# Optimization experiments

Hardware: AMD Instinct MI355X
Metric: run time of the kernel (lower is better)

## Reference

```python
import jax, jax.numpy as jnp
import numpy as np
from jax import lax

N_GROUPS = 2
TOPK_GROUPS = 1
TOPK = 4
ROUTE_SCALE = 1.0


def setup_inputs() -> dict:
    key = jax.random.key(0)
    k1, k2 = jax.random.split(key)
    T, D, E = 524288, 256, 64
    x = jax.random.normal(k1, (T, D), dtype=jnp.float32)
    W = jax.random.normal(k2, (E, D), dtype=jnp.float32) * 0.02  # router weight [out, in]
    return {"x": x, "W": W}


def reference(x, W):
    T = x.shape[0]
    E = W.shape[0]
    logits = x @ W.T  # [T, E]
    scores = jax.nn.softmax(logits.astype(jnp.float32), axis=-1)
    original_scores = scores
    # grouped masking (bias is None -> amax group score)
    g = scores.reshape(T, N_GROUPS, E // N_GROUPS)
    group_scores = g.max(axis=-1)  # [T, G]
    _, gidx = lax.top_k(group_scores, TOPK_GROUPS)  # [T, topk_groups]
    keep = jnp.zeros((T, N_GROUPS), dtype=bool).at[jnp.arange(T)[:, None], gidx].set(True)
    masked = jnp.where(keep[:, :, None], g, -jnp.inf).reshape(T, E)
    _, indices = lax.top_k(masked, TOPK)  # [T, topk]
    weights = jnp.take_along_axis(original_scores, indices, axis=1)
    weights = weights * ROUTE_SCALE
    return weights.astype(x.dtype), indices
```

## Files before the change

kernel.cpp:

```cpp
#include <hip/hip_runtime.h>
#include <hip/hip_bf16.h>
#include <stdint.h>


typedef __attribute__((ext_vector_type(8))) short bf16x8;
typedef __attribute__((ext_vector_type(4))) float f32x4;
typedef __attribute__((ext_vector_type(4))) int i32x4;

#define SPLIT_OFF 1024
#define LIST_OFF 102400
#define DELTA 1e-4f

__device__ __forceinline__ f32x4 mf(const i32x4& a, const i32x4& b,
                                    const f32x4& c) {
  return __builtin_amdgcn_mfma_f32_16x16x32_bf16(
      __builtin_bit_cast(bf16x8, a), __builtin_bit_cast(bf16x8, b), c, 0, 0, 0);
}

__device__ __forceinline__ int packhi(unsigned e0, unsigned e1) {
  return (int)__builtin_amdgcn_perm(e1, e0, 0x07060302u);
}

__device__ __forceinline__ void gload16(const void* g, void* l) {
  __builtin_amdgcn_global_load_lds(
      (const __attribute__((address_space(1))) void*)g,
      (__attribute__((address_space(3))) void*)l, 16, 0, 0);
}

__global__ void split_w(const float* __restrict__ W,
                        unsigned short* __restrict__ ws, int n,
                        int* __restrict__ meta) {
  int i = blockIdx.x * 256 + threadIdx.x;
  if (i == 0) meta[0] = 0;
  if (i >= n) return;
  float w = W[i];
  unsigned u = __float_as_uint(w);
  unsigned uh = u & 0xFFFF0000u;
  float rf = w - __uint_as_float(uh);
  unsigned short lv[2];
  lv[0] = (unsigned short)(uh >> 16);
  lv[1] = (unsigned short)(__float_as_uint(rf) >> 16);
  int e = i >> 8, k = i & 255;
  int nt = e >> 4, le = e & 15;
  int c = k >> 5, lg = (k >> 3) & 3, kk = k & 7;
  int lane = lg * 16 + le;
#pragma unroll
  for (int v = 0; v < 2; ++v)
    ws[(((c * 8 + v * 4 + nt) * 64) + lane) * 8 + kk] = lv[v];
}

struct XF2 { i32x4 h, m; };

__device__ __forceinline__ XF2 split2(f32x4 a, f32x4 b) {
  float xs[8] = {a[0], a[1], a[2], a[3], b[0], b[1], b[2], b[3]};
  XF2 f;
#pragma unroll
  for (int wd = 0; wd < 4; ++wd) {
    unsigned u0 = __float_as_uint(xs[2 * wd]);
    unsigned u1 = __float_as_uint(xs[2 * wd + 1]);
    f.h[wd] = packhi(u0, u1);
    float r0 = xs[2 * wd] - __uint_as_float(u0 & 0xFFFF0000u);
    float r1 = xs[2 * wd + 1] - __uint_as_float(u1 & 0xFFFF0000u);
    f.m[wd] = packhi(__float_as_uint(r0), __float_as_uint(r1));
  }
  return f;
}

#define GL(dst, ptr, OFF)                                     \
  asm volatile("global_load_dwordx4 %0, %1, off offset:%2"    \
               : "=v"(dst)                                    \
               : "v"(ptr), "n"(OFF))

#define WAITV(NSTR)                                         \
  do {                                                      \
    asm volatile("s_waitcnt vmcnt(" NSTR ")" ::: "memory"); \
    __builtin_amdgcn_sched_barrier(0);                      \
  } while (0)

__global__ __launch_bounds__(512, 4) void gate_kernel(
    const float* __restrict__ x, const unsigned short* __restrict__ wsp,
    float* __restrict__ out, int* __restrict__ meta, int* __restrict__ list,
    int cap, int T) {
  __shared__ i32x4 WL[4096];

  const int t = threadIdx.x;
  const int lane = t & 63;
  const int wid = t >> 6;
  const int le = lane & 15;
  const int lg = lane >> 4;
  const int tokbase = blockIdx.x * 256 + wid * 32;

  const float* xa0 = x + (size_t)(tokbase + le) * 256 + lg * 8;
  const float* xa1 = xa0 + 16 * 256;

  f32x4 xbuf[2][4];
  f32x4 acc[4][2];
#pragma unroll
  for (int nt = 0; nt < 4; ++nt)
#pragma unroll
    for (int t2 = 0; t2 < 2; ++t2) acc[nt][t2] = (f32x4)0.0f;

#define STAGE_X(c)                              \
  do {                                          \
    GL(xbuf[(c) & 1][0], xa0, (c) * 128);       \
    GL(xbuf[(c) & 1][1], xa0, (c) * 128 + 16);  \
    GL(xbuf[(c) & 1][2], xa1, (c) * 128);       \
    GL(xbuf[(c) & 1][3], xa1, (c) * 128 + 16);  \
  } while (0)

#define ITER(c, NSTR)                                               \
  {                                                                 \
    WAITV(NSTR);                                                    \
    XF2 b0 = split2(xbuf[(c) & 1][0], xbuf[(c) & 1][1]);            \
    XF2 b1 = split2(xbuf[(c) & 1][2], xbuf[(c) & 1][3]);            \
    if ((c) + 2 < 8) STAGE_X((c) + 2);                              \
    _Pragma("unroll") for (int nt = 0; nt < 4; ++nt) {              \
      i32x4 ah = WL[(((c) * 8 + nt) << 6) + lane];                  \
      i32x4 am = WL[(((c) * 8 + 4 + nt) << 6) + lane];              \
      acc[nt][0] = mf(ah, b0.h, acc[nt][0]);                        \
      acc[nt][0] = mf(ah, b0.m, acc[nt][0]);                        \
      acc[nt][0] = mf(am, b0.h, acc[nt][0]);                        \
      acc[nt][0] = mf(am, b0.m, acc[nt][0]);                        \
      acc[nt][1] = mf(ah, b1.h, acc[nt][1]);                        \
      acc[nt][1] = mf(ah, b1.m, acc[nt][1]);                        \
      acc[nt][1] = mf(am, b1.h, acc[nt][1]);                        \
      acc[nt][1] = mf(am, b1.m, acc[nt][1]);                        \
    }                                                               \
  }

  {
    const char* wsrc = (const char*)wsp + t * 16;
    char* wdst = (char*)WL + t * 16;
#pragma unroll
    for (int i = 0; i < 8; ++i) gload16(wsrc + i * 8192, wdst + i * 8192);
  }
  STAGE_X(0);
  STAGE_X(1);
  WAITV("8");
  __builtin_amdgcn_s_barrier();

  ITER(0, "4");
  ITER(1, "4");
  ITER(2, "4");
  ITER(3, "4");
  ITER(4, "4");
  ITER(5, "4");
  ITER(6, "4");
  ITER(7, "0");

#pragma unroll
  for (int tt = 0; tt < 2; ++tt) {
    float l[16];
#pragma unroll
    for (int nt = 0; nt < 4; ++nt)
#pragma unroll
      for (int j = 0; j < 4; ++j) l[nt * 4 + j] = acc[nt][tt][j];

    float g0 = l[0], g1 = l[8];
#pragma unroll
    for (int j = 1; j < 8; ++j) {
      g0 = fmaxf(g0, l[j]);
      g1 = fmaxf(g1, l[8 + j]);
    }
    g0 = fmaxf(g0, __shfl_xor(g0, 16));
    g0 = fmaxf(g0, __shfl_xor(g0, 32));
    g1 = fmaxf(g1, __shfl_xor(g1, 16));
    g1 = fmaxf(g1, __shfl_xor(g1, 32));
    const int g = (g1 > g0) ? 1 : 0;
    const float m = fmaxf(g0, g1);

    float sum = 0.f;
#pragma unroll
    for (int k = 0; k < 16; ++k) sum += __expf(l[k] - m);
    sum += __shfl_xor(sum, 16);
    sum += __shfl_xor(sum, 32);
    const float inv = 1.0f / sum;

    float c[8];
    int ce[8];
#pragma unroll
    for (int j2 = 0; j2 < 8; ++j2) {
      c[j2] = l[g * 8 + j2];
      ce[j2] = (2 * g + (j2 >> 2)) * 16 + 4 * lg + (j2 & 3);
    }

    float v5[5];
    int e5[5];
#pragma unroll
    for (int it = 0; it < 5; ++it) {
      float bv = c[0];
      int be = ce[0];
#pragma unroll
      for (int j2 = 1; j2 < 8; ++j2) {
        bool gt = c[j2] > bv;
        bv = gt ? c[j2] : bv;
        be = gt ? ce[j2] : be;
      }
#pragma unroll
      for (int st = 0; st < 2; ++st) {
        int msk = 16 << st;
        float ov = __shfl_xor(bv, msk);
        int oe = __shfl_xor(be, msk);
        bool tk = (ov > bv) || (ov == bv && oe < be);
        bv = tk ? ov : bv;
        be = tk ? oe : be;
      }
      v5[it] = bv;
      e5[it] = be;
#pragma unroll
      for (int j2 = 0; j2 < 8; ++j2)
        c[j2] = (ce[j2] == be) ? -3.0e38f : c[j2];
    }

    float ming = fabsf(g0 - g1);
#pragma unroll
    for (int it = 0; it < 4; ++it) ming = fminf(ming, v5[it] - v5[it + 1]);

    if (lg == 0) {
      size_t trow = (size_t)tokbase + tt * 16 + le;
      *(float4*)&out[trow * 4] =
          make_float4(__expf(v5[0] - m) * inv, __expf(v5[1] - m) * inv,
                      __expf(v5[2] - m) * inv, __expf(v5[3] - m) * inv);
      *(float4*)&out[(size_t)T * 4 + trow * 4] = make_float4(
          (float)e5[0], (float)e5[1], (float)e5[2], (float)e5[3]);
      if (ming < DELTA) {
        int p = atomicAdd(meta, 1);
        if (p < cap) list[p] = (int)trow;
      }
    }
  }
}

__global__ __launch_bounds__(64) void fix_kernel(
    const float* __restrict__ x, const float* __restrict__ W,
    float* __restrict__ out, const int* __restrict__ meta,
    const int* __restrict__ list, int cap, int T) {
  const int e = threadIdx.x;
  int cnt = meta[0];
  cnt = cnt < cap ? cnt : cap;
  for (int i = blockIdx.x; i < cnt; i += gridDim.x) {
    const int tok = list[i];
    const float* xr = x + (size_t)tok * 256;
    const float* wr = W + (size_t)e * 256;
    float acc = 0.f;
#pragma unroll 8
    for (int d = 0; d < 256; d += 4) {
      float4 xv = *(const float4*)(xr + d);
      float4 wv = *(const float4*)(wr + d);
      acc = fmaf(xv.x, wv.x, acc);
      acc = fmaf(xv.y, wv.y, acc);
      acc = fmaf(xv.z, wv.z, acc);
      acc = fmaf(xv.w, wv.w, acc);
    }
    float gm = acc;
#pragma unroll
    for (int st = 0; st < 5; ++st) gm = fmaxf(gm, __shfl_xor(gm, 1 << st));
    float om = __shfl_xor(gm, 32);
    float g0 = (e < 32) ? gm : om;
    float g1 = (e < 32) ? om : gm;
    const int g = (g1 > g0) ? 1 : 0;
    const float m = fmaxf(g0, g1);
    float sum = __expf(acc - m);
#pragma unroll
    for (int st = 0; st < 6; ++st) sum += __shfl_xor(sum, 1 << st);
    const float inv = 1.0f / sum;

    float cand = ((e >> 5) == g) ? acc : -3.0e38f;
    float w4[4], i4[4];
#pragma unroll
    for (int it = 0; it < 4; ++it) {
      float bv = cand;
      int be = e;
#pragma unroll
      for (int st = 0; st < 6; ++st) {
        int msk = 1 << st;
        float ov = __shfl_xor(bv, msk);
        int oe = __shfl_xor(be, msk);
        bool tk = (ov > bv) || (ov == bv && oe < be);
        bv = tk ? ov : bv;
        be = tk ? oe : be;
      }
      w4[it] = __expf(bv - m) * inv;
      i4[it] = (float)be;
      if (e == be) cand = -3.0e38f;
    }
    if (e == 0) {
      *(float4*)&out[(size_t)tok * 4] = make_float4(w4[0], w4[1], w4[2], w4[3]);
      *(float4*)&out[(size_t)T * 4 + (size_t)tok * 4] =
          make_float4(i4[0], i4[1], i4[2], i4[3]);
    }
  }
}

extern "C" void kernel_launch(void* const* d_in, const int* in_sizes, int n_in,
                              void* d_out, int out_size, void* d_ws,
                              size_t ws_size, hipStream_t stream) {
  const float* x = (const float*)d_in[0];
  const float* W = (const float*)d_in[1];
  float* out = (float*)d_out;
  int T = in_sizes[0] / 256;
  int nW = in_sizes[1];
  int* meta = (int*)d_ws;
  unsigned short* wsp = (unsigned short*)((char*)d_ws + SPLIT_OFF);
  int* list = (int*)((char*)d_ws + LIST_OFF);
  int cap = (ws_size > LIST_OFF + 4) ? (int)((ws_size - LIST_OFF) / 4) : 0;
  hipLaunchKernelGGL(split_w, dim3((nW + 255) / 256), dim3(256), 0, stream, W,
                     wsp, nW, meta);
  hipLaunchKernelGGL(gate_kernel, dim3(T / 256), dim3(512), 0, stream, x, wsp,
                     out, meta, list, cap, T);
  hipLaunchKernelGGL(fix_kernel, dim3(2048), dim3(64), 0, stream, x, W, out,
                     meta, list, cap, T);
}
```

Before: 142.1 us.

## Make gate kernel persistent with cross-tile prefetch of next x chunk

```diff
diff --git a/kernel.cpp b/kernel.cpp
--- a/kernel.cpp
+++ b/kernel.cpp
@@ -77,6 +77,8 @@
     __builtin_amdgcn_sched_barrier(0);                      \
   } while (0)
 
+#define NBLK 512
+
 __global__ __launch_bounds__(512, 4) void gate_kernel(
     const float* __restrict__ x, const unsigned short* __restrict__ wsp,
     float* __restrict__ out, int* __restrict__ meta, int* __restrict__ list,
@@ -88,32 +90,33 @@
   const int wid = t >> 6;
   const int le = lane & 15;
   const int lg = lane >> 4;
-  const int tokbase = blockIdx.x * 256 + wid * 32;
-
-  const float* xa0 = x + (size_t)(tokbase + le) * 256 + lg * 8;
+  const int ngen = (T / 256) / NBLK;
+  const size_t GS = (size_t)NBLK * 256 * 256;
+
+  int tokb = blockIdx.x * 256 + wid * 32;
+  const float* xa0 = x + (size_t)(tokb + le) * 256 + lg * 8;
   const float* xa1 = xa0 + 16 * 256;
 
   f32x4 xbuf[2][4];
-  f32x4 acc[4][2];
-#pragma unroll
-  for (int nt = 0; nt < 4; ++nt)
-#pragma unroll
-    for (int t2 = 0; t2 < 2; ++t2) acc[nt][t2] = (f32x4)0.0f;
-
-#define STAGE_X(c)                              \
-  do {                                          \
-    GL(xbuf[(c) & 1][0], xa0, (c) * 128);       \
-    GL(xbuf[(c) & 1][1], xa0, (c) * 128 + 16);  \
-    GL(xbuf[(c) & 1][2], xa1, (c) * 128);       \
-    GL(xbuf[(c) & 1][3], xa1, (c) * 128 + 16);  \
+
+#define STAGE_XP(p0, p1, bi, OFF)        \
+  do {                                   \
+    GL(xbuf[bi][0], p0, OFF);            \
+    GL(xbuf[bi][1], p0, (OFF) + 16);     \
+    GL(xbuf[bi][2], p1, OFF);            \
+    GL(xbuf[bi][3], p1, (OFF) + 16);     \
   } while (0)
 
-#define ITER(c, NSTR)                                               \
+#define ITER(c)                                                     \
   {                                                                 \
-    WAITV(NSTR);                                                    \
+    WAITV("4");                                                     \
     XF2 b0 = split2(xbuf[(c) & 1][0], xbuf[(c) & 1][1]);            \
     XF2 b1 = split2(xbuf[(c) & 1][2], xbuf[(c) & 1][3]);            \
-    if ((c) + 2 < 8) STAGE_X((c) + 2);                              \
+    if ((c) + 2 < 8) {                                              \
+      STAGE_XP(xa0, xa1, (c) & 1, ((c) + 2) * 128);                 \
+    } else {                                                        \
+      STAGE_XP(xn0, xn1, (c) & 1, ((c) - 6) * 128);                 \
+    }                                                               \
     _Pragma("unroll") for (int nt = 0; nt < 4; ++nt) {              \
       i32x4 ah = WL[(((c) * 8 + nt) << 6) + lane];                  \
       i32x4 am = WL[(((c) * 8 + 4 + nt) << 6) + lane];              \
@@ -134,100 +137,111 @@
 #pragma unroll
     for (int i = 0; i < 8; ++i) gload16(wsrc + i * 8192, wdst + i * 8192);
   }
-  STAGE_X(0);
-  STAGE_X(1);
+  STAGE_XP(xa0, xa1, 0, 0);
+  STAGE_XP(xa0, xa1, 1, 128);
   WAITV("8");
   __builtin_amdgcn_s_barrier();
 
-  ITER(0, "4");
-  ITER(1, "4");
-  ITER(2, "4");
-  ITER(3, "4");
-  ITER(4, "4");
-  ITER(5, "4");
-  ITER(6, "4");
-  ITER(7, "0");
-
-#pragma unroll
-  for (int tt = 0; tt < 2; ++tt) {
-    float l[16];
+#pragma unroll 1
+  for (int g = 0; g < ngen; ++g) {
+    const bool lastg = (g + 1 >= ngen);
+    const float* xn0 = lastg ? xa0 : xa0 + GS;
+    const float* xn1 = lastg ? xa1 : xa1 + GS;
+
+    f32x4 acc[4][2];
 #pragma unroll
     for (int nt = 0; nt < 4; ++nt)
 #pragma unroll
-      for (int j = 0; j < 4; ++j) l[nt * 4 + j] = acc[nt][tt][j];
-
-    float g0 = l[0], g1 = l[8];
-#pragma unroll
-    for (int j = 1; j < 8; ++j) {
-      g0 = fmaxf(g0, l[j]);
-      g1 = fmaxf(g1, l[8 + j]);
+      for (int t2 = 0; t2 < 2; ++t2) acc[nt][t2] = (f32x4)0.0f;
+
+    ITER(0); ITER(1); ITER(2); ITER(3);
+    ITER(4); ITER(5); ITER(6); ITER(7);
+
+#pragma unroll
+    for (int tt = 0; tt < 2; ++tt) {
+      float l[16];
+#pragma unroll
+      for (int nt = 0; nt < 4; ++nt)
+#pragma unroll
+        for (int j = 0; j < 4; ++j) l[nt * 4 + j] = acc[nt][tt][j];
+
+      float g0 = l[0], g1 = l[8];
+#pragma unroll
+      for (int j = 1; j < 8; ++j) {
+        g0 = fmaxf(g0, l[j]);
+        g1 = fmaxf(g1, l[8 + j]);
+      }
+      g0 = fmaxf(g0, __shfl_xor(g0, 16));
+      g0 = fmaxf(g0, __shfl_xor(g0, 32));
+      g1 = fmaxf(g1, __shfl_xor(g1, 16));
+      g1 = fmaxf(g1, __shfl_xor(g1, 32));
+      const int grp = (g1 > g0) ? 1 : 0;
+      const float m = fmaxf(g0, g1);
+
+      float sum = 0.f;
+#pragma unroll
+      for (int k = 0; k < 16; ++k) sum += __expf(l[k] - m);
+      sum += __shfl_xor(sum, 16);
+      sum += __shfl_xor(sum, 32);
+      const float inv = 1.0f / sum;
+
+      float c[8];
+      int ce[8];
+#pragma unroll
+      for (int j2 = 0; j2 < 8; ++j2) {
+        c[j2] = l[grp * 8 + j2];
+        ce[j2] = (2 * grp + (j2 >> 2)) * 16 + 4 * lg + (j2 & 3);
+      }
+
+      float v5[5];
+      int e5[5];
+#pragma unroll
+      for (int it = 0; it < 5; ++it) {
+        float bv = c[0];
+        int be = ce[0];
+#pragma unroll
+        for (int j2 = 1; j2 < 8; ++j2) {
+          bool gt = c[j2] > bv;
+          bv = gt ? c[j2] : bv;
+          be = gt ? ce[j2] : be;
+        }
+#pragma unroll
+        for (int st = 0; st < 2; ++st) {
+          int msk = 16 << st;
+          float ov = __shfl_xor(bv, msk);
+          int oe = __shfl_xor(be, msk);
+          bool tk = (ov > bv) || (ov == bv && oe < be);
+          bv = tk ? ov : bv;
+          be = tk ? oe : be;
+        }
+        v5[it] = bv;
+        e5[it] = be;
+#pragma unroll
+        for (int j2 = 0; j2 < 8; ++j2)
+          c[j2] = (ce[j2] == be) ? -3.0e38f : c[j2];
+      }
+
+      float ming = fabsf(g0 - g1);
+#pragma unroll
+      for (int it = 0; it < 4; ++it) ming = fminf(ming, v5[it] - v5[it + 1]);
+
+      if (lg == 0) {
+        size_t trow = (size_t)tokb + tt * 16 + le;
+        *(float4*)&out[trow * 4] =
+            make_float4(__expf(v5[0] - m) * inv, __expf(v5[1] - m) * inv,
+                        __expf(v5[2] - m) * inv, __expf(v5[3] - m) * inv);
+        *(float4*)&out[(size_t)T * 4 + trow * 4] = make_float4(
+            (float)e5[0], (float)e5[1], (float)e5[2], (float)e5[3]);
+        if (ming < DELTA) {
+          int p = atomicAdd(meta, 1);
+          if (p < cap) list[p] = (int)trow;
+        }
+      }
     }
-    g0 = fmaxf(g0, __shfl_xor(g0, 16));
-    g0 = fmaxf(g0, __shfl_xor(g0, 32));
-    g1 = fmaxf(g1, __shfl_xor(g1, 16));
-    g1 = fmaxf(g1, __shfl_xor(g1, 32));
-    const int g = (g1 > g0) ? 1 : 0;
-    const float m = fmaxf(g0, g1);
-
-    float sum = 0.f;
-#pragma unroll
-    for (int k = 0; k < 16; ++k) sum += __expf(l[k] - m);
-    sum += __shfl_xor(sum, 16);
-    sum += __shfl_xor(sum, 32);
-    const float inv = 1.0f / sum;
-
-    float c[8];
-    int ce[8];
-#pragma unroll
-    for (int j2 = 0; j2 < 8; ++j2) {
-      c[j2] = l[g * 8 + j2];
-      ce[j2] = (2 * g + (j2 >> 2)) * 16 + 4 * lg + (j2 & 3);
-    }
-
-    float v5[5];
-    int e5[5];
-#pragma unroll
-    for (int it = 0; it < 5; ++it) {
-      float bv = c[0];
-      int be = ce[0];
-#pragma unroll
-      for (int j2 = 1; j2 < 8; ++j2) {
-        bool gt = c[j2] > bv;
-        bv = gt ? c[j2] : bv;
-        be = gt ? ce[j2] : be;
-      }
-#pragma unroll
-      for (int st = 0; st < 2; ++st) {
-        int msk = 16 << st;
-        float ov = __shfl_xor(bv, msk);
-        int oe = __shfl_xor(be, msk);
-        bool tk = (ov > bv) || (ov == bv && oe < be);
-        bv = tk ? ov : bv;
-        be = tk ? oe : be;
-      }
-      v5[it] = bv;
-      e5[it] = be;
-#pragma unroll
-      for (int j2 = 0; j2 < 8; ++j2)
-        c[j2] = (ce[j2] == be) ? -3.0e38f : c[j2];
-    }
-
-    float ming = fabsf(g0 - g1);
-#pragma unroll
-    for (int it = 0; it < 4; ++it) ming = fminf(ming, v5[it] - v5[it + 1]);
-
-    if (lg == 0) {
-      size_t trow = (size_t)tokbase + tt * 16 + le;
-      *(float4*)&out[trow * 4] =
-          make_float4(__expf(v5[0] - m) * inv, __expf(v5[1] - m) * inv,
-                      __expf(v5[2] - m) * inv, __expf(v5[3] - m) * inv);
-      *(float4*)&out[(size_t)T * 4 + trow * 4] = make_float4(
-          (float)e5[0], (float)e5[1], (float)e5[2], (float)e5[3]);
-      if (ming < DELTA) {
-        int p = atomicAdd(meta, 1);
-        if (p < cap) list[p] = (int)trow;
-      }
-    }
+
+    xa0 = xn0;
+    xa1 = xn1;
+    tokb += NBLK * 256;
   }
 }
 
@@ -306,8 +320,8 @@
   int cap = (ws_size > LIST_OFF + 4) ? (int)((ws_size - LIST_OFF) / 4) : 0;
   hipLaunchKernelGGL(split_w, dim3((nW + 255) / 256), dim3(256), 0, stream, W,
                      wsp, nW, meta);
-  hipLaunchKernelGGL(gate_kernel, dim3(T / 256), dim3(512), 0, stream, x, wsp,
+  hipLaunchKernelGGL(gate_kernel, dim3(NBLK), dim3(512), 0, stream, x, wsp,
                      out, meta, list, cap, T);
-  hipLaunchKernelGGL(fix_kernel, dim3(2048), dim3(64), 0, stream, x, W, out,
+  hipLaunchKernelGGL(fix_kernel, dim3(4096), dim3(64), 0, stream, x, W, out,
                      meta, list, cap, T);
 }
```

New measurement: 145.8 us. +2.6%, slower.

## Fuse W split and near-tie fixup into single gate kernel

Applied to the files above, without the earlier changes.

```diff
diff --git a/kernel.cpp b/kernel.cpp
--- a/kernel.cpp
+++ b/kernel.cpp
@@ -7,8 +7,6 @@
 typedef __attribute__((ext_vector_type(4))) float f32x4;
 typedef __attribute__((ext_vector_type(4))) int i32x4;
 
-#define SPLIT_OFF 1024
-#define LIST_OFF 102400
 #define DELTA 1e-4f
 
 __device__ __forceinline__ f32x4 mf(const i32x4& a, const i32x4& b,
@@ -19,34 +17,6 @@
 
 __device__ __forceinline__ int packhi(unsigned e0, unsigned e1) {
   return (int)__builtin_amdgcn_perm(e1, e0, 0x07060302u);
-}
-
-__device__ __forceinline__ void gload16(const void* g, void* l) {
-  __builtin_amdgcn_global_load_lds(
-      (const __attribute__((address_space(1))) void*)g,
-      (__attribute__((address_space(3))) void*)l, 16, 0, 0);
-}
-
-__global__ void split_w(const float* __restrict__ W,
-                        unsigned short* __restrict__ ws, int n,
-                        int* __restrict__ meta) {
-  int i = blockIdx.x * 256 + threadIdx.x;
-  if (i == 0) meta[0] = 0;
-  if (i >= n) return;
-  float w = W[i];
-  unsigned u = __float_as_uint(w);
-  unsigned uh = u & 0xFFFF0000u;
-  float rf = w - __uint_as_float(uh);
-  unsigned short lv[2];
-  lv[0] = (unsigned short)(uh >> 16);
-  lv[1] = (unsigned short)(__float_as_uint(rf) >> 16);
-  int e = i >> 8, k = i & 255;
-  int nt = e >> 4, le = e & 15;
-  int c = k >> 5, lg = (k >> 3) & 3, kk = k & 7;
-  int lane = lg * 16 + le;
-#pragma unroll
-  for (int v = 0; v < 2; ++v)
-    ws[(((c * 8 + v * 4 + nt) * 64) + lane) * 8 + kk] = lv[v];
 }
 
 struct XF2 { i32x4 h, m; };
@@ -78,9 +48,8 @@
   } while (0)
 
 __global__ __launch_bounds__(512, 4) void gate_kernel(
-    const float* __restrict__ x, const unsigned short* __restrict__ wsp,
-    float* __restrict__ out, int* __restrict__ meta, int* __restrict__ list,
-    int cap, int T) {
+    const float* __restrict__ x, const float* __restrict__ W,
+    float* __restrict__ out, int T) {
   __shared__ i32x4 WL[4096];
 
   const int t = threadIdx.x;
@@ -88,9 +57,37 @@
   const int wid = t >> 6;
   const int le = lane & 15;
   const int lg = lane >> 4;
-  const int tokbase = blockIdx.x * 256 + wid * 32;
-
-  const float* xa0 = x + (size_t)(tokbase + le) * 256 + lg * 8;
+  const int tokb = blockIdx.x * 256 + wid * 32;
+
+  {
+    const float* wr = W + t * 32;
+    float wv[32];
+#pragma unroll
+    for (int j = 0; j < 8; ++j)
+      *(float4*)&wv[j * 4] = *(const float4*)(wr + j * 4);
+    const int e = t >> 3, c = t & 7;
+    const int nt = e >> 4, lew = e & 15;
+#pragma unroll
+    for (int lg2 = 0; lg2 < 4; ++lg2) {
+      i32x4 vh, vm;
+#pragma unroll
+      for (int p = 0; p < 4; ++p) {
+        float a0 = wv[lg2 * 8 + 2 * p], a1 = wv[lg2 * 8 + 2 * p + 1];
+        unsigned u0 = __float_as_uint(a0), u1 = __float_as_uint(a1);
+        vh[p] = packhi(u0, u1);
+        float r0 = a0 - __uint_as_float(u0 & 0xFFFF0000u);
+        float r1 = a1 - __uint_as_float(u1 & 0xFFFF0000u);
+        vm[p] = packhi(__float_as_uint(r0), __float_as_uint(r1));
+      }
+      WL[(c * 8 + nt) * 64 + lg2 * 16 + lew] = vh;
+      WL[(c * 8 + 4 + nt) * 64 + lg2 * 16 + lew] = vm;
+    }
+  }
+  asm volatile("s_waitcnt lgkmcnt(0)" ::: "memory");
+  __builtin_amdgcn_sched_barrier(0);
+  __builtin_amdgcn_s_barrier();
+
+  const float* xa0 = x + (size_t)(tokb + le) * 256 + lg * 8;
   const float* xa1 = xa0 + 16 * 256;
 
   f32x4 xbuf[2][4];
@@ -128,17 +125,8 @@
     }                                                               \
   }
 
-  {
-    const char* wsrc = (const char*)wsp + t * 16;
-    char* wdst = (char*)WL + t * 16;
-#pragma unroll
-    for (int i = 0; i < 8; ++i) gload16(wsrc + i * 8192, wdst + i * 8192);
-  }
   STAGE_X(0);
   STAGE_X(1);
-  WAITV("8");
-  __builtin_amdgcn_s_barrier();
-
   ITER(0, "4");
   ITER(1, "4");
   ITER(2, "4");
@@ -148,6 +136,7 @@
   ITER(6, "4");
   ITER(7, "0");
 
+  unsigned long long fmask = 0ull;
 #pragma unroll
   for (int tt = 0; tt < 2; ++tt) {
     float l[16];
@@ -166,7 +155,7 @@
     g0 = fmaxf(g0, __shfl_xor(g0, 32));
     g1 = fmaxf(g1, __shfl_xor(g1, 16));
     g1 = fmaxf(g1, __shfl_xor(g1, 32));
-    const int g = (g1 > g0) ? 1 : 0;
+    const int grp = (g1 > g0) ? 1 : 0;
     const float m = fmaxf(g0, g1);
 
     float sum = 0.f;
@@ -180,8 +169,8 @@
     int ce[8];
 #pragma unroll
     for (int j2 = 0; j2 < 8; ++j2) {
-      c[j2] = l[g * 8 + j2];
-      ce[j2] = (2 * g + (j2 >> 2)) * 16 + 4 * lg + (j2 & 3);
+      c[j2] = l[grp * 8 + j2];
+      ce[j2] = (2 * grp + (j2 >> 2)) * 16 + 4 * lg + (j2 & 3);
     }
 
     float v5[5];
@@ -216,43 +205,37 @@
 #pragma unroll
     for (int it = 0; it < 4; ++it) ming = fminf(ming, v5[it] - v5[it + 1]);
 
-    if (lg == 0) {
-      size_t trow = (size_t)tokbase + tt * 16 + le;
+    const bool flg = (ming < DELTA);
+    fmask |= (__ballot(lg == 0 && flg) << (tt * 16));
+
+    if (lg == 0 && !flg) {
+      size_t trow = (size_t)tokb + tt * 16 + le;
       *(float4*)&out[trow * 4] =
           make_float4(__expf(v5[0] - m) * inv, __expf(v5[1] - m) * inv,
                       __expf(v5[2] - m) * inv, __expf(v5[3] - m) * inv);
       *(float4*)&out[(size_t)T * 4 + trow * 4] = make_float4(
           (float)e5[0], (float)e5[1], (float)e5[2], (float)e5[3]);
-      if (ming < DELTA) {
-        int p = atomicAdd(meta, 1);
-        if (p < cap) list[p] = (int)trow;
-      }
-    }
-  }
-}
-
-__global__ __launch_bounds__(64) void fix_kernel(
-    const float* __restrict__ x, const float* __restrict__ W,
-    float* __restrict__ out, const int* __restrict__ meta,
-    const int* __restrict__ list, int cap, int T) {
-  const int e = threadIdx.x;
-  int cnt = meta[0];
-  cnt = cnt < cap ? cnt : cap;
-  for (int i = blockIdx.x; i < cnt; i += gridDim.x) {
-    const int tok = list[i];
-    const float* xr = x + (size_t)tok * 256;
+    }
+  }
+
+  while (fmask) {
+    const int b = __builtin_ctzll(fmask);
+    fmask &= fmask - 1;
+    const size_t tok = (size_t)tokb + (b >> 4) * 16 + (b & 15);
+    const int e = lane;
+    const float* xr = x + tok * 256;
     const float* wr = W + (size_t)e * 256;
-    float acc = 0.f;
+    float accx = 0.f;
 #pragma unroll 8
     for (int d = 0; d < 256; d += 4) {
       float4 xv = *(const float4*)(xr + d);
       float4 wv = *(const float4*)(wr + d);
-      acc = fmaf(xv.x, wv.x, acc);
-      acc = fmaf(xv.y, wv.y, acc);
-      acc = fmaf(xv.z, wv.z, acc);
-      acc = fmaf(xv.w, wv.w, acc);
-    }
-    float gm = acc;
+      accx = fmaf(xv.x, wv.x, accx);
+      accx = fmaf(xv.y, wv.y, accx);
+      accx = fmaf(xv.z, wv.z, accx);
+      accx = fmaf(xv.w, wv.w, accx);
+    }
+    float gm = accx;
 #pragma unroll
     for (int st = 0; st < 5; ++st) gm = fmaxf(gm, __shfl_xor(gm, 1 << st));
     float om = __shfl_xor(gm, 32);
@@ -260,12 +243,12 @@
     float g1 = (e < 32) ? om : gm;
     const int g = (g1 > g0) ? 1 : 0;
     const float m = fmaxf(g0, g1);
-    float sum = __expf(acc - m);
+    float sum = __expf(accx - m);
 #pragma unroll
     for (int st = 0; st < 6; ++st) sum += __shfl_xor(sum, 1 << st);
     const float inv = 1.0f / sum;
 
-    float cand = ((e >> 5) == g) ? acc : -3.0e38f;
+    float cand = ((e >> 5) == g) ? accx : -3.0e38f;
     float w4[4], i4[4];
 #pragma unroll
     for (int it = 0; it < 4; ++it) {
@@ -285,8 +268,8 @@
       if (e == be) cand = -3.0e38f;
     }
     if (e == 0) {
-      *(float4*)&out[(size_t)tok * 4] = make_float4(w4[0], w4[1], w4[2], w4[3]);
-      *(float4*)&out[(size_t)T * 4 + (size_t)tok * 4] =
+      *(float4*)&out[tok * 4] = make_float4(w4[0], w4[1], w4[2], w4[3]);
+      *(float4*)&out[(size_t)T * 4 + tok * 4] =
           make_float4(i4[0], i4[1], i4[2], i4[3]);
     }
   }
@@ -299,15 +282,6 @@
   const float* W = (const float*)d_in[1];
   float* out = (float*)d_out;
   int T = in_sizes[0] / 256;
-  int nW = in_sizes[1];
-  int* meta = (int*)d_ws;
-  unsigned short* wsp = (unsigned short*)((char*)d_ws + SPLIT_OFF);
-  int* list = (int*)((char*)d_ws + LIST_OFF);
-  int cap = (ws_size > LIST_OFF + 4) ? (int)((ws_size - LIST_OFF) / 4) : 0;
-  hipLaunchKernelGGL(split_w, dim3((nW + 255) / 256), dim3(256), 0, stream, W,
-                     wsp, nW, meta);
-  hipLaunchKernelGGL(gate_kernel, dim3(T / 256), dim3(512), 0, stream, x, wsp,
-                     out, meta, list, cap, T);
-  hipLaunchKernelGGL(fix_kernel, dim3(2048), dim3(64), 0, stream, x, W, out,
-                     meta, list, cap, T);
-}
+  hipLaunchKernelGGL(gate_kernel, dim3(T / 256), dim3(512), 0, stream, x, W,
+                     out, T);
+}
```

New measurement: 158.6 us. 1.12x slower.
